# Optimization experiments

Measured on AMD Instinct MI355X. Metric: run time of the kernel, lower is better.

## Reference

```python
import jax, jax.numpy as jnp
import numpy as np
from jax import lax

B, H, W = 2, 960, 1280
K = 1024            # max_keypoints
P = 256             # num_pairs (BAD descriptor dim)
NUM_SCALES = 3
DIFF_ITERS = 3
KAPPA = 0.05
TAU = 0.2           # explicit FED step size (stable < 0.25)
DET_THRESHOLD = 0.001
AKAZE_NMS = 5       # detector-internal NMS window
NMS_WIN = 2 * 3 + 1 # pipeline NMS window (nms_radius=3)
ORI_PATCH = 15
ORI_SIGMA = 2.5
SINK_ITERS = 20
EPSILON = 1.0
UNUSED_SCORE = 1.0
MAX_RADIUS = 5

def _conv(x, k):
    return lax.conv_general_dilated(x, k, (1, 1), 'SAME', dimension_numbers=('NCHW', 'OIHW', 'NCHW'))

_sob = np.array([[-1., 0., 1.], [-2., 0., 2.], [-1., 0., 1.]], np.float32) / 8.0
KX = jnp.asarray(_sob)[None, None]
KY = jnp.asarray(_sob.T)[None, None]
_d2 = np.array([[0., 0., 0.], [1., -2., 1.], [0., 0., 0.]], np.float32)
KXX = jnp.asarray(_d2)[None, None]
KYY = jnp.asarray(_d2.T)[None, None]

# Gaussian weighting kernel for orientation estimation
_c = np.arange(ORI_PATCH, dtype=np.float32) - (ORI_PATCH - 1) / 2.0
_gy, _gx = np.meshgrid(_c, _c, indexing='ij')
_g = np.exp(-(_gx ** 2 + _gy ** 2) / (2.0 * ORI_SIGMA ** 2))
GK = jnp.asarray((_g / _g.sum()).astype(np.float32))[None, None]

# Box-average kernel bank: one normalized box filter per radius 0..MAX_RADIUS
_bc = np.arange(-MAX_RADIUS, MAX_RADIUS + 1, dtype=np.float32)
_by, _bx = np.meshgrid(_bc, _bc, indexing='ij')
_rv = np.arange(MAX_RADIUS + 1, dtype=np.float32)[:, None, None]
_bm = ((np.abs(_by) <= _rv) & (np.abs(_bx) <= _rv)).astype(np.float32)
BOX_BANK = jnp.asarray((_bm / (2.0 * _rv + 1.0) ** 2)[:, None])  # [R+1,1,11,11]

def _shifts(a):
    p = jnp.pad(a, ((0, 0), (0, 0), (1, 1), (1, 1)), mode='edge')
    return p[:, :, :-2, 1:-1], p[:, :, 2:, 1:-1], p[:, :, 1:-1, :-2], p[:, :, 1:-1, 2:]

def _fed_step(L):
    # One explicit Perona-Malik (FED) nonlinear diffusion step
    Lx = _conv(L, KX); Ly = _conv(L, KY)
    g = 1.0 / (1.0 + (Lx * Lx + Ly * Ly) / (KAPPA * KAPPA))
    Ln, Ls, Lw, Le = _shifts(L)
    gn, gs, gw, ge = _shifts(g)
    flux = 0.5 * ((g + gn) * (Ln - L) + (g + gs) * (Ls - L) + (g + gw) * (Lw - L) + (g + ge) * (Le - L))
    return L + TAU * flux

def _maxpool(s, win):
    return lax.reduce_window(s, -jnp.inf, lax.max, (1, win, win), (1, 1, 1), 'SAME')

def _akaze(img):
    # Multi-scale FED diffusion -> Hessian determinant response + orientation map
    L = img
    resp = jnp.zeros((B, H, W), img.dtype)
    for _s in range(NUM_SCALES):
        for _i in range(DIFF_ITERS):
            L = _fed_step(L)
        Lxx = _conv(L, KXX); Lyy = _conv(L, KYY); Lxy = _conv(_conv(L, KX), KY)
        resp = jnp.maximum(resp, (Lxx * Lyy - Lxy * Lxy)[:, 0])
    resp = jnp.where(resp > DET_THRESHOLD, resp, 0.0)
    resp = resp * (resp >= _maxpool(resp, AKAZE_NMS) - 1e-7).astype(resp.dtype)
    gxs = _conv(_conv(img, KX), GK)[:, 0]
    gys = _conv(_conv(img, KY), GK)[:, 0]
    theta = jnp.arctan2(gys, gxs)  # [B,H,W]
    return resp, theta

def _select(resp):
    # Pipeline-level maxpool NMS + top-K selection, pad invalid with (-1,-1)
    mask = (resp >= _maxpool(resp, NMS_WIN) - 1e-7).astype(resp.dtype)
    s = resp * mask
    s = jnp.where(s > 0.0, s, 0.0)
    tk, idx = lax.top_k(s.reshape(B, -1), K)
    y = (idx // W).astype(jnp.float32)
    x = (idx % W).astype(jnp.float32)
    valid = (tk > 0.0).astype(jnp.float32)
    kpts = jnp.where(valid[..., None] > 0.5, jnp.stack([y, x], -1), -1.0)
    return kpts, tk * valid, valid

def _bad(img, kpts, theta, valid, offsets, radii, thresholds):
    # Orientation-aware BAD: box-averaged intensity differences at rotated pair offsets
    bank = _conv(img, BOX_BANK)  # [B,R+1,H,W]
    yc = jnp.clip(kpts[..., 0], 0.0, H - 1.0)
    xc = jnp.clip(kpts[..., 1], 0.0, W - 1.0)
    yi = jnp.round(yc).astype(jnp.int32); xi = jnp.round(xc).astype(jnp.int32)
    th = jax.vmap(lambda m, a, b: m[a, b])(theta, yi, xi)  # [B,K] nearest-sampled orientation
    c = jnp.cos(th)[..., None]; s = jnp.sin(th)[..., None]
    ox1, oy1, ox2, oy2 = offsets[:, 0], offsets[:, 1], offsets[:, 2], offsets[:, 3]
    px1 = xc[..., None] + c * ox1 - s * oy1
    py1 = yc[..., None] + s * ox1 + c * oy1
    px2 = xc[..., None] + c * ox2 - s * oy2
    py2 = yc[..., None] + s * ox2 + c * oy2
    rb = jnp.broadcast_to(radii[None, :], (K, P))
    def samp(px, py):
        xi_ = jnp.clip(jnp.round(px), 0, W - 1).astype(jnp.int32)
        yi_ = jnp.clip(jnp.round(py), 0, H - 1).astype(jnp.int32)
        return jax.vmap(lambda bk, a, b: bk[rb, a, b])(bank, yi_, xi_)  # [B,K,P]
    v = (samp(px1, py1) - samp(px2, py2)) - thresholds[None, None, :]
    v = v * valid[..., None]
    n = jnp.linalg.norm(v, axis=-1, keepdims=True)
    return v / (n + 1e-8)

def _sinkhorn(d1, d2):
    sq1 = jnp.sum(d1 * d1, -1); sq2 = jnp.sum(d2 * d2, -1)
    dist2 = sq1[:, :, None] + sq2[:, None, :] - 2.0 * jnp.einsum('bip,bjp->bij', d1, d2)
    dist = jnp.sqrt(jnp.maximum(dist2, 0.0) + 1e-12)
    Z = jnp.full((B, K + 1, K + 1), UNUSED_SCORE, d1.dtype)
    Z = Z.at[:, :K, :K].set(-dist) / EPSILON
    norm = -jnp.log(2.0 * K)
    log_mu = jnp.concatenate([jnp.zeros(K, Z.dtype), jnp.log(float(K)) * jnp.ones(1, Z.dtype)]) + norm
    log_nu = log_mu
    def body(carry, _):
        u, v = carry
        u = log_mu[None] - jax.nn.logsumexp(Z + v[:, None, :], axis=2)
        v = log_nu[None] - jax.nn.logsumexp(Z + u[:, :, None], axis=1)
        return (u, v), None
    (u, v), _ = lax.scan(body, (jnp.zeros((B, K + 1), Z.dtype), jnp.zeros((B, K + 1), Z.dtype)), None, length=SINK_ITERS)
    return jnp.exp(Z + u[:, :, None] + v[:, None, :] - norm)  # [B,K+1,K+1]

def _forward(img1, img2, offsets, thresholds, radii):
    r1, t1 = _akaze(img1)
    r2, t2 = _akaze(img2)
    k1, s1, v1 = _select(r1)
    k2, s2, v2 = _select(r2)
    d1 = _bad(img1, k1, t1, v1, offsets, radii, thresholds)
    d2 = _bad(img2, k2, t2, v2, offsets, radii, thresholds)
    probs = _sinkhorn(d1, d2)
    return k1, k2, probs

def setup_inputs():
    key = jax.random.key(0)
    k1, k2, k3, k4, k5 = jax.random.split(key, 5)
    img1 = jax.random.uniform(k1, (B, 1, H, W), jnp.float32)
    img2 = jax.random.uniform(k2, (B, 1, H, W), jnp.float32)
    offsets = jax.random.uniform(k3, (P, 4), jnp.float32, -16.0, 16.0)  # box_params - 16
    thresholds = 0.05 * jax.random.normal(k5, (P,), jnp.float32)
    radii = jax.random.randint(k4, (P,), 0, MAX_RADIUS + 1, jnp.int32)
    return {'img1': img1, 'img2': img2, 'offsets': offsets, 'thresholds': thresholds, 'radii': radii}

def reference(img1, img2, offsets, thresholds, radii):
    return _forward(img1, img2, offsets, thresholds, radii)
```

## Files before the change

kernel.cpp:

```cpp
#include <hip/hip_runtime.h>
#include <hip/hip_fp16.h>
#include <math.h>

typedef unsigned long long u64;
typedef unsigned int u32;

#define Hh 960
#define Ww 1280
#define Bb 2
#define Kk 1024
#define Pp 256
#define KP1 1025
#define NSEG 4
#define LISTCAP 131072
#define PR 28
#define PS 57
#define ZLD 1040
static const size_t ZB = (size_t)KP1*ZLD;

static const size_t HWp = (size_t)Hh * Ww;
static const size_t PLn = HWp * Bb;

#define TAUf 0.2f
#define NMS_EPS 1e-7f
#define DET_T 0.001f
#define NORMV (-7.6246189861593985f)
#define LOGKV (6.9314718055994531f)

__constant__ float WR[6] = {1.0f, 1.0f/9.0f, 1.0f/25.0f, 1.0f/49.0f, 1.0f/81.0f, 1.0f/121.0f};

__device__ __forceinline__ int imin(int a,int b){return a<b?a:b;}
__device__ __forceinline__ int imax(int a,int b){return a>b?a:b;}

__global__ __launch_bounds__(256) void fed_step(const float* __restrict__ src, float* __restrict__ dst){
  __shared__ float Lt[36][37];
  __shared__ float Gt[34][35];
  const int bx = blockIdx.x*32, by = blockIdx.y*32, b = blockIdx.z;
  const float* S = src + (size_t)b*HWp;
  float* D = dst + (size_t)b*HWp;
  const int t = threadIdx.y*32 + threadIdx.x;
  for (int i=t;i<36*36;i+=256){
    int ly=i/36, lx=i-ly*36;
    int gy=by+ly-2, gx=bx+lx-2;
    Lt[ly][lx] = (gy>=0 && gy<Hh && gx>=0 && gx<Ww) ? S[(size_t)gy*Ww+gx] : 0.0f;
  }
  __syncthreads();
  const float k2 = (float)(0.05*0.05);
  for (int i=t;i<34*34;i+=256){
    int ly=i/34, lx=i-ly*34;
    int Ly=ly+1, Lx=lx+1;
    float sx = (-Lt[Ly-1][Lx-1]+Lt[Ly-1][Lx+1]
                -2.0f*Lt[Ly][Lx-1]+2.0f*Lt[Ly][Lx+1]
                -Lt[Ly+1][Lx-1]+Lt[Ly+1][Lx+1])*0.125f;
    float sy = (-Lt[Ly-1][Lx-1]-2.0f*Lt[Ly-1][Lx]-Lt[Ly-1][Lx+1]
                +Lt[Ly+1][Lx-1]+2.0f*Lt[Ly+1][Lx]+Lt[Ly+1][Lx+1])*0.125f;
    Gt[ly][lx] = 1.0f/(1.0f + (sx*sx+sy*sy)/k2);
  }
  __syncthreads();
  for (int r=0;r<4;++r){
    int oy=threadIdx.y + r*8, ox=threadIdx.x;
    int gy=by+oy, gx=bx+ox;
    if (gy>=Hh || gx>=Ww) continue;
    int gyn=imax(gy-1,0), gys=imin(gy+1,Hh-1), gxw=imax(gx-1,0), gxe=imin(gx+1,Ww-1);
    float Lc=Lt[oy+2][ox+2];
    float Ln=Lt[gyn-by+2][ox+2];
    float Ls=Lt[gys-by+2][ox+2];
    float Lw=Lt[oy+2][gxw-bx+2];
    float Le=Lt[oy+2][gxe-bx+2];
    float gc=Gt[oy+1][ox+1];
    float gn=Gt[gyn-by+1][ox+1];
    float gs=Gt[gys-by+1][ox+1];
    float gw=Gt[oy+1][gxw-bx+1];
    float ge=Gt[oy+1][gxe-bx+1];
    float flux = 0.5f*((gc+gn)*(Ln-Lc) + (gc+gs)*(Ls-Lc) + (gc+gw)*(Lw-Lc) + (gc+ge)*(Le-Lc));
    D[(size_t)gy*Ww+gx] = Lc + TAUf*flux;
  }
}

__global__ __launch_bounds__(256) void response_kernel(const float* __restrict__ src, float* __restrict__ resp, int first){
  __shared__ float Lt[36][37];
  __shared__ float Sx[34][35];
  const int bx = blockIdx.x*32, by = blockIdx.y*32, b = blockIdx.z;
  const float* S = src + (size_t)b*HWp;
  float* R = resp + (size_t)b*HWp;
  const int t = threadIdx.y*32 + threadIdx.x;
  for (int i=t;i<36*36;i+=256){
    int ly=i/36, lx=i-ly*36;
    int gy=by+ly-2, gx=bx+lx-2;
    Lt[ly][lx] = (gy>=0 && gy<Hh && gx>=0 && gx<Ww) ? S[(size_t)gy*Ww+gx] : 0.0f;
  }
  __syncthreads();
  for (int i=t;i<34*34;i+=256){
    int ly=i/34, lx=i-ly*34;
    int gy=by+ly-1, gx=bx+lx-1;
    float v=0.0f;
    if (gy>=0 && gy<Hh && gx>=0 && gx<Ww){
      int Ly=ly+1, Lx=lx+1;
      v = (-Lt[Ly-1][Lx-1]+Lt[Ly-1][Lx+1]
           -2.0f*Lt[Ly][Lx-1]+2.0f*Lt[Ly][Lx+1]
           -Lt[Ly+1][Lx-1]+Lt[Ly+1][Lx+1])*0.125f;
    }
    Sx[ly][lx]=v;
  }
  __syncthreads();
  for (int r=0;r<4;++r){
    int oy=threadIdx.y + r*8, ox=threadIdx.x;
    int gy=by+oy, gx=bx+ox;
    if (gy>=Hh || gx>=Ww) continue;
    int Ly=oy+2, Lx=ox+2;
    float Lxx = Lt[Ly][Lx-1]-2.0f*Lt[Ly][Lx]+Lt[Ly][Lx+1];
    float Lyy = Lt[Ly-1][Lx]-2.0f*Lt[Ly][Lx]+Lt[Ly+1][Lx];
    int Sy=oy+1, Sxi=ox+1;
    float Lxy = (-Sx[Sy-1][Sxi-1]-2.0f*Sx[Sy-1][Sxi]-Sx[Sy-1][Sxi+1]
                 +Sx[Sy+1][Sxi-1]+2.0f*Sx[Sy+1][Sxi]+Sx[Sy+1][Sxi+1])*0.125f;
    float det = Lxx*Lyy - Lxy*Lxy;
    size_t id=(size_t)gy*Ww+gx;
    R[id] = first ? fmaxf(det,0.0f) : fmaxf(R[id], det);
  }
}

__global__ __launch_bounds__(256) void detect_compact(const float* __restrict__ resp,
                                                      u64* __restrict__ lists,
                                                      int* __restrict__ cnt, int segbase){
  const int TS=42;
  __shared__ float Tt[TS][TS+1];
  __shared__ float H5[TS][40];
  __shared__ float Ss[38][39];
  __shared__ u64 keys[1024];
  __shared__ int lcnt, gbase;
  const int bx = blockIdx.x*32, by = blockIdx.y*32, b = blockIdx.z;
  const float* S = resp + (size_t)b*HWp;
  const int t = threadIdx.y*32 + threadIdx.x;
  if (t==0) lcnt=0;
  for (int i=t;i<TS*TS;i+=256){
    int ly=i/TS, lx=i-ly*TS;
    int gy=by+ly-5, gx=bx+lx-5;
    float v = (gy>=0 && gy<Hh && gx>=0 && gx<Ww) ? S[(size_t)gy*Ww+gx] : 0.0f;
    Tt[ly][lx] = (v>DET_T) ? v : 0.0f;
  }
  __syncthreads();
  for (int i=t;i<42*38;i+=256){
    int y=i/38, x=i-(i/38)*38;
    float m=Tt[y][x];
    m=fmaxf(m,Tt[y][x+1]); m=fmaxf(m,Tt[y][x+2]);
    m=fmaxf(m,Tt[y][x+3]); m=fmaxf(m,Tt[y][x+4]);
    H5[y][x]=m;
  }
  __syncthreads();
  for (int i=t;i<38*38;i+=256){
    int y=i/38, x=i-(i/38)*38;
    float m=H5[y][x];
    m=fmaxf(m,H5[y+1][x]); m=fmaxf(m,H5[y+2][x]);
    m=fmaxf(m,H5[y+3][x]); m=fmaxf(m,H5[y+4][x]);
    float c=Tt[y+2][x+2];
    Ss[y][x]=(c>=m-NMS_EPS)?c:0.0f;
  }
  __syncthreads();
  const int seg=segbase+b;
  for (int r=0;r<4;++r){
    int oy=threadIdx.y + r*8, ox=threadIdx.x;
    int gy=by+oy, gx=bx+ox;
    bool pos=false; u64 key=0;
    if (gy<Hh && gx<Ww){
      float v=Ss[oy+3][ox+3];
      if (v>0.0f){
        float m=0.0f;
        #pragma unroll
        for(int dy=0;dy<7;dy++)
          #pragma unroll
          for(int dx=0;dx<7;dx++)
            m=fmaxf(m,Ss[oy+dy][ox+dx]);
        if (v>=m-NMS_EPS){
          u32 idx=(u32)(gy*Ww+gx);
          key=((u64)__float_as_uint(v)<<32)|(u64)(0xFFFFFFFFu-idx);
          pos=true;
        }
      }
    }
    u64 mask=__ballot(pos);
    if (mask){
      int lane=t&63;
      int leader=__ffsll((long long)mask)-1;
      int base=0;
      if (lane==leader) base=atomicAdd(&lcnt,__popcll(mask));
      base=__shfl(base,leader);
      if (pos){
        int rk=__popcll(mask & ((1ULL<<lane)-1ULL));
        keys[base+rk]=key;
      }
    }
  }
  __syncthreads();
  if (t==0 && lcnt>0) gbase=atomicAdd(&cnt[seg*64], lcnt);
  __syncthreads();
  int n=lcnt;
  for (int i=t;i<n;i+=256){
    int p=gbase+i;
    if (p<LISTCAP) lists[(size_t)seg*LISTCAP+p]=keys[i];
  }
}

__device__ __forceinline__ void segbar(int* bar, int* gen, int seg, int target){
  __syncthreads();
  if(threadIdx.x==0){
    __threadfence();
    int old=atomicAdd(&bar[seg*16],1);
    if(old==7){
      atomicExch(&bar[seg*16],0);
      atomicAdd(&gen[seg*16],1);
    } else {
      while(__hip_atomic_load(&gen[seg*16],__ATOMIC_ACQUIRE,__HIP_MEMORY_SCOPE_AGENT)<target){
        __builtin_amdgcn_s_sleep(8);
      }
    }
    __threadfence();
  }
  __syncthreads();
}

__global__ __launch_bounds__(256) void topk_all(const u64* __restrict__ lists, const int* __restrict__ cnt,
                          u32* __restrict__ ghist, int* __restrict__ krem, int* __restrict__ takeAll,
                          u64* __restrict__ prefix, u64* __restrict__ Tf,
                          u64* __restrict__ selbuf, int* __restrict__ selcnt,
                          int* __restrict__ bar, int* __restrict__ gen){
  const int seg=blockIdx.y, bid=blockIdx.x, tid=threadIdx.x;
  __shared__ u32 h[256];
  __shared__ int tash;
  __shared__ u64 pfxsh;
  const int n=imin(cnt[seg*64],LISTCAP);
  const u64* L=lists+(size_t)seg*LISTCAP;
  int target=0;
  for(int rd=0;rd<8;rd++){
    if(tid==0){
      tash=(rd>0)?__hip_atomic_load(&takeAll[seg],__ATOMIC_RELAXED,__HIP_MEMORY_SCOPE_AGENT):0;
      pfxsh=(rd>0)?__hip_atomic_load(&prefix[seg],__ATOMIC_RELAXED,__HIP_MEMORY_SCOPE_AGENT):0ULL;
    }
    h[tid]=0;
    __syncthreads();
    if(!tash){
      int shift=56-8*rd;
      u64 maskHi=(rd==0)?0ULL:(~0ULL<<(shift+8));
      u64 pfx=pfxsh;
      for(int i=bid*256+tid;i<n;i+=8*256){
        u64 k=L[i];
        if((k&maskHi)==pfx) atomicAdd(&h[(int)((k>>shift)&255ULL)],1u);
      }
      __syncthreads();
      if(h[tid]) atomicAdd(&ghist[seg*256+tid],h[tid]);
    }
    segbar(bar,gen,seg,++target);
    if(bid==0){
      h[tid]=__hip_atomic_load(&ghist[seg*256+tid],__ATOMIC_RELAXED,__HIP_MEMORY_SCOPE_AGENT);
      __syncthreads();
      if(tid==0){
        if(rd==0){
          krem[seg]=Kk;
          __hip_atomic_store(&prefix[seg],0ULL,__ATOMIC_RELEASE,__HIP_MEMORY_SCOPE_AGENT);
          __hip_atomic_store(&takeAll[seg],(n<=Kk)?1:0,__ATOMIC_RELEASE,__HIP_MEMORY_SCOPE_AGENT);
        }
        int taNow=__hip_atomic_load(&takeAll[seg],__ATOMIC_RELAXED,__HIP_MEMORY_SCOPE_AGENT);
        if(taNow){
          if(rd==7) __hip_atomic_store(&Tf[seg],1ULL,__ATOMIC_RELEASE,__HIP_MEMORY_SCOPE_AGENT);
        } else {
          int kr=krem[seg];
          int acc=0,b2=255;
          for(;b2>0;--b2){ int c2=(int)h[b2]; if(acc+c2>=kr) break; acc+=c2; }
          int shift=56-8*rd;
          u64 pf=__hip_atomic_load(&prefix[seg],__ATOMIC_RELAXED,__HIP_MEMORY_SCOPE_AGENT);
          pf|=((u64)(u32)b2)<<shift;
          __hip_atomic_store(&prefix[seg],pf,__ATOMIC_RELEASE,__HIP_MEMORY_SCOPE_AGENT);
          krem[seg]=kr-acc;
          if(rd==7) __hip_atomic_store(&Tf[seg],pf,__ATOMIC_RELEASE,__HIP_MEMORY_SCOPE_AGENT);
        }
      }
      __syncthreads();
      ghist[seg*256+tid]=0u;
    }
    segbar(bar,gen,seg,++target);
  }
  u64 T=__hip_atomic_load(&Tf[seg],__ATOMIC_RELAXED,__HIP_MEMORY_SCOPE_AGENT);
  for(int i0=bid*256;i0<n;i0+=8*256){
    int i=i0+tid;
    bool sel=false; u64 k=0;
    if(i<n){ k=L[i]; sel=(k>=T); }
    u64 mask=__ballot(sel);
    if(mask){
      int lane=tid&63;
      int leader=__ffsll((long long)mask)-1;
      int base=0;
      if(lane==leader) base=atomicAdd(&selcnt[seg*64],__popcll(mask));
      base=__shfl(base,leader);
      if(sel){
        int p=base+__popcll(mask & ((1ULL<<lane)-1ULL));
        if(p<Kk) selbuf[(size_t)seg*Kk+p]=k;
      }
    }
  }
}

__global__ __launch_bounds__(1024) void finalize_kernel(const u64* __restrict__ selbuf, const int* __restrict__ selcnt,
                                int* __restrict__ kyi, int* __restrict__ kxi, float* __restrict__ kval,
                                float* __restrict__ outp){
  int seg=blockIdx.x, tid=threadIdx.x;
  __shared__ u64 a[1024];
  int n=selcnt[seg*64]; if(n>Kk)n=Kk;
  a[tid]=(tid<n)?selbuf[(size_t)seg*Kk+tid]:0ULL;
  __syncthreads();
  for(int k=2;k<=1024;k<<=1){
    for(int j=k>>1;j>0;j>>=1){
      int ixj=tid^j;
      if(ixj>tid){
        u64 x=a[tid], y=a[ixj];
        bool desc=((tid&k)==0);
        if(desc ? (x<y) : (x>y)){ a[tid]=y; a[ixj]=x; }
      }
      __syncthreads();
    }
  }
  u64 key=a[tid];
  bool val=(key!=0ULL);
  u32 idx=0xFFFFFFFFu-(u32)(key&0xFFFFFFFFULL);
  int y= val ? (int)(idx/Ww) : 0;
  int x= val ? (int)(idx%Ww) : 0;
  int mi=seg*Kk+tid;
  kyi[mi]=y; kxi[mi]=x; kval[mi]= val?1.0f:0.0f;
  int imi=seg>>1, bb=seg&1;
  float* ko=outp + (size_t)imi*(Bb*Kk*2) + ((size_t)bb*Kk+tid)*2;
  ko[0]= val ? (float)y : -1.0f;
  ko[1]= val ? (float)x : -1.0f;
}

__global__ void init_weights(float* wn){
  if(threadIdx.x==0 && blockIdx.x==0){
    double w[15]; double S=0.0;
    for(int i=0;i<15;i++){ double c=(double)i-7.0; w[i]=exp(-(c*c)/(2.0*2.5*2.5)); S+=w[i]; }
    for(int i=0;i<15;i++) wn[i]=(float)(w[i]/S);
  }
}

__device__ __forceinline__ float ldz(const float* __restrict__ img,int y,int x){
  return (y>=0&&y<Hh&&x>=0&&x<Ww)?img[(size_t)y*Ww+x]:0.0f;
}

__global__ __launch_bounds__(64) void orient_kernel(const float* __restrict__ img1, const float* __restrict__ img2,
                              const int* __restrict__ kyi, const int* __restrict__ kxi,
                              const float* __restrict__ wn, float* __restrict__ kth){
  int seg=blockIdx.y, ki=blockIdx.x, lane=threadIdx.x;
  __shared__ float w15[15];
  if(lane<15) w15[lane]=wn[lane];
  __syncthreads();
  const float* img=(seg<2?img1:img2)+(size_t)(seg&1)*HWp;
  int mi=seg*Kk+ki;
  int yc=kyi[mi], xc=kxi[mi];
  float ax=0.0f, ay=0.0f;
  for(int tp=lane;tp<225;tp+=64){
    int du=tp/15-7, dv=tp-(tp/15)*15-7;
    int yy=yc+du, xx=xc+dv;
    if(yy<0||yy>=Hh||xx<0||xx>=Ww) continue;
    float p00=ldz(img,yy-1,xx-1), p01=ldz(img,yy-1,xx), p02=ldz(img,yy-1,xx+1);
    float p10=ldz(img,yy,xx-1),                          p12=ldz(img,yy,xx+1);
    float p20=ldz(img,yy+1,xx-1), p21=ldz(img,yy+1,xx), p22=ldz(img,yy+1,xx+1);
    float sx=(-p00+p02-2.0f*p10+2.0f*p12-p20+p22)*0.125f;
    float sy=(-p00-2.0f*p01-p02+p20+2.0f*p21+p22)*0.125f;
    float wgt=w15[du+7]*w15[dv+7];
    ax=fmaf(wgt,sx,ax); ay=fmaf(wgt,sy,ay);
  }
  for(int o=32;o;o>>=1){ ax+=__shfl_down(ax,o); ay+=__shfl_down(ay,o); }
  if(lane==0) kth[mi]=atan2f(ay,ax);
}

__global__ __launch_bounds__(256) void bad_kernel(const float* __restrict__ img1, const float* __restrict__ img2,
                           const float* __restrict__ offs, const float* __restrict__ thrv,
                           const int* __restrict__ rad,
                           const int* __restrict__ kyi, const int* __restrict__ kxi,
                           const float* __restrict__ kval, const float* __restrict__ kth,
                           float* __restrict__ d1, float* __restrict__ d2,
                           float* __restrict__ sq1, float* __restrict__ sq2){
  __shared__ float sat[PS+1][PS+2];
  __shared__ float sm[4];
  __shared__ float nsh;
  int seg=blockIdx.y, ki=blockIdx.x, p=threadIdx.x;
  const float* img=(seg<2?img1:img2)+(size_t)(seg&1)*HWp;
  int mi=seg*Kk+ki;
  int yci=kyi[mi], xci=kxi[mi];
  for (int i=p;i<PS+1;i+=256){ sat[0][i]=0.0f; sat[i][0]=0.0f; }
  if (p==0) sat[0][PS]=0.0f;
  for (int i=p;i<PS*PS;i+=256){
    int ly=i/PS, lx=i-ly*PS;
    int gy=yci-PR+ly, gx=xci-PR+lx;
    sat[ly+1][lx+1]=(gy>=0&&gy<Hh&&gx>=0&&gx<Ww)?img[(size_t)gy*Ww+gx]:0.0f;
  }
  __syncthreads();
  if (p<PS){
    float run=0.0f;
    for(int x=1;x<=PS;x++){ run+=sat[p+1][x]; sat[p+1][x]=run; }
  }
  __syncthreads();
  if (p<PS){
    float run=0.0f;
    for(int y=1;y<=PS;y++){ run+=sat[y][p+1]; sat[y][p+1]=run; }
  }
  __syncthreads();
  float yc=(float)yci, xc=(float)xci;
  float th=kth[mi];
  float c=cosf(th), s=sinf(th);
  float ox1=offs[p*4+0], oy1=offs[p*4+1], ox2=offs[p*4+2], oy2=offs[p*4+3];
  int r=rad[p];
  float w=WR[r];
  float px1=xc+c*ox1-s*oy1, py1=yc+s*ox1+c*oy1;
  float px2=xc+c*ox2-s*oy2, py2=yc+s*ox2+c*oy2;
  auto boxl=[&](float px,float py,int r_)->float{
    float rx=rintf(px), ry=rintf(py);
    int xi=(int)fminf(fmaxf(rx,0.0f),(float)(Ww-1));
    int yi=(int)fminf(fmaxf(ry,0.0f),(float)(Hh-1));
    int lx=xi-(xci-PR), ly=yi-(yci-PR);
    int y2=ly+r_+1, y1=ly-r_, x2=lx+r_+1, x1=lx-r_;
    return sat[y2][x2]-sat[y1][x2]-sat[y2][x1]+sat[y1][x1];
  };
  float s1=boxl(px1,py1,r)*w;
  float s2=boxl(px2,py2,r)*w;
  float v=(s1-s2-thrv[p])*kval[mi];
  float t=v*v;
  for(int o=32;o;o>>=1) t+=__shfl_down(t,o);
  if((p&63)==0) sm[p>>6]=t;
  __syncthreads();
  if(p==0) nsh=sqrtf(sm[0]+sm[1]+sm[2]+sm[3]);
  __syncthreads();
  float dv=v/(nsh+1e-8f);
  float* dd=(seg<2?d1:d2);
  dd[((size_t)(seg&1)*Kk+ki)*Pp+p]=dv;
  float t2=dv*dv;
  for(int o=32;o;o>>=1) t2+=__shfl_down(t2,o);
  __syncthreads();
  if((p&63)==0) sm[p>>6]=t2;
  __syncthreads();
  if(p==0){ float* sq=(seg<2?sq1:sq2); sq[(size_t)(seg&1)*Kk+ki]=sm[0]+sm[1]+sm[2]+sm[3]; }
}

__global__ __launch_bounds__(256) void dist_kernel(const float* __restrict__ d1, const float* __restrict__ d2,
                            const float* __restrict__ sq1, const float* __restrict__ sq2,
                            float* __restrict__ Zm, float* __restrict__ Zt){
  int b=blockIdx.z;
  int i0=blockIdx.y*64, j0=blockIdx.x*64;
  int tid=threadIdx.x;
  int tx=tid&15, ty=tid>>4;
  __shared__ float Ast[64][68], Bst[64][68];
  const float* D1=d1+(size_t)b*Kk*Pp;
  const float* D2=d2+(size_t)b*Kk*Pp;
  float acc[4][4]={};
  for(int p0=0;p0<Pp;p0+=64){
    for(int i=tid;i<64*16;i+=256){
      int row=i>>4, c4=(i&15)<<2;
      float4 va=*reinterpret_cast<const float4*>(&D1[(size_t)(i0+row)*Pp+p0+c4]);
      float4 vb=*reinterpret_cast<const float4*>(&D2[(size_t)(j0+row)*Pp+p0+c4]);
      Ast[c4+0][row]=va.x; Ast[c4+1][row]=va.y; Ast[c4+2][row]=va.z; Ast[c4+3][row]=va.w;
      Bst[c4+0][row]=vb.x; Bst[c4+1][row]=vb.y; Bst[c4+2][row]=vb.z; Bst[c4+3][row]=vb.w;
    }
    __syncthreads();
    #pragma unroll 8
    for(int kk=0;kk<64;++kk){
      float4 av=*reinterpret_cast<const float4*>(&Ast[kk][ty*4]);
      float4 bv=*reinterpret_cast<const float4*>(&Bst[kk][tx*4]);
      acc[0][0]=fmaf(av.x,bv.x,acc[0][0]); acc[0][1]=fmaf(av.x,bv.y,acc[0][1]);
      acc[0][2]=fmaf(av.x,bv.z,acc[0][2]); acc[0][3]=fmaf(av.x,bv.w,acc[0][3]);
      acc[1][0]=fmaf(av.y,bv.x,acc[1][0]); acc[1][1]=fmaf(av.y,bv.y,acc[1][1]);
      acc[1][2]=fmaf(av.y,bv.z,acc[1][2]); acc[1][3]=fmaf(av.y,bv.w,acc[1][3]);
      acc[2][0]=fmaf(av.z,bv.x,acc[2][0]); acc[2][1]=fmaf(av.z,bv.y,acc[2][1]);
      acc[2][2]=fmaf(av.z,bv.z,acc[2][2]); acc[2][3]=fmaf(av.z,bv.w,acc[2][3]);
      acc[3][0]=fmaf(av.w,bv.x,acc[3][0]); acc[3][1]=fmaf(av.w,bv.y,acc[3][1]);
      acc[3][2]=fmaf(av.w,bv.z,acc[3][2]); acc[3][3]=fmaf(av.w,bv.w,acc[3][3]);
    }
    __syncthreads();
  }
  int gi=i0+ty*4, gj=j0+tx*4;
  float si[4], sj[4];
  #pragma unroll
  for(int i=0;i<4;i++){ si[i]=sq1[b*Kk+gi+i]; sj[i]=sq2[b*Kk+gj+i]; }
  #pragma unroll
  for(int i=0;i<4;i++){
    #pragma unroll
    for(int j=0;j<4;j++){
      float dd=si[i]+sj[j]-2.0f*acc[i][j];
      float dist=sqrtf(fmaxf(dd,0.0f)+1e-12f);
      Zm[(size_t)b*ZB+(size_t)(gi+i)*ZLD+(gj+j)]=-dist;
      Zt[(size_t)b*ZB+(size_t)(gj+j)*ZLD+(gi+i)]=-dist;
    }
  }
}

__global__ void zborder_kernel(float* __restrict__ Zm, float* __restrict__ Zt){
  int i=blockIdx.x*256+threadIdx.x;
  if(i>=Bb*KP1) return;
  int b=i/KP1, j=i-(i/KP1)*KP1;
  size_t base=(size_t)b*ZB;
  Zm[base+(size_t)j*ZLD+Kk]=1.0f;
  Zm[base+(size_t)Kk*ZLD+j]=1.0f;
  Zt[base+(size_t)j*ZLD+Kk]=1.0f;
  Zt[base+(size_t)Kk*ZLD+j]=1.0f;
  for(int c=KP1;c<ZLD;c++){
    Zm[base+(size_t)j*ZLD+c]=-1.0e30f;
    Zt[base+(size_t)j*ZLD+c]=-1.0e30f;
  }
}

__global__ void expz_kernel(const float* __restrict__ Zm, const float* __restrict__ Zt,
                            __half* __restrict__ Em, __half* __restrict__ Et){
  size_t q=(size_t)blockIdx.x*256+threadIdx.x;
  const size_t tot4=(size_t)Bb*ZB/4;
  if(q>=2*tot4) return;
  const float* src=(q<tot4)?Zm:Zt;
  __half* dst=(q<tot4)?Em:Et;
  size_t j=(q<tot4)?q:q-tot4;
  float4 z=reinterpret_cast<const float4*>(src)[j];
  __half2 a=__floats2half2_rn(expf(z.x),expf(z.y));
  __half2 b=__floats2half2_rn(expf(z.z),expf(z.w));
  reinterpret_cast<__half2*>(dst)[2*j]=a;
  reinterpret_cast<__half2*>(dst)[2*j+1]=b;
}

__global__ void init_euv(float* __restrict__ euv, float* __restrict__ evv){
  int i=blockIdx.x*256+threadIdx.x;
  if(i>=Bb*ZLD) return;
  int j=i-(i/ZLD)*ZLD;
  evv[i]=(j<KP1)?1.0f:0.0f;
  euv[i]=0.0f;
}

struct H4{ __half2 a, b; };
__global__ __launch_bounds__(256) void sink_gemv(const __half* __restrict__ E,
        const float* __restrict__ evin, float* __restrict__ euout, float* __restrict__ uout){
  int row=blockIdx.x*4+(threadIdx.x>>6);
  if(row>=Bb*KP1) return;
  int b=row/KP1, i=row-b*KP1;
  int lane=threadIdx.x&63;
  const H4* e4=reinterpret_cast<const H4*>(E+((size_t)b*KP1+i)*ZLD);
  const float4* v4=reinterpret_cast<const float4*>(evin+(size_t)b*ZLD);
  float s=0.0f;
  for(int j=lane;j<ZLD/4;j+=64){
    H4 e=e4[j]; float4 v=v4[j];
    float2 ea=__half22float2(e.a), eb=__half22float2(e.b);
    s=fmaf(ea.x,v.x,s); s=fmaf(ea.y,v.y,s);
    s=fmaf(eb.x,v.z,s); s=fmaf(eb.y,v.w,s);
  }
  for(int o=32;o;o>>=1) s+=__shfl_down(s,o);
  if(lane==0){
    float lm,elm;
    if(i<Kk){ lm=NORMV; elm=4.8828125e-4f; }
    else    { lm=LOGKV+NORMV; elm=0.5f; }
    euout[(size_t)b*ZLD+i]=elm/s;
    uout [(size_t)b*ZLD+i]=lm-logf(s);
  }
}

__global__ void probs_kernel(const float* __restrict__ Zm, const float* __restrict__ uu,
                             const float* __restrict__ vv, float* __restrict__ outp){
  size_t i=(size_t)blockIdx.x*256+threadIdx.x;
  const size_t tot=(size_t)Bb*KP1*KP1;
  if(i>=tot) return;
  size_t b=i/((size_t)KP1*KP1);
  size_t rem=i-b*(size_t)KP1*KP1;
  int rr=(int)(rem/KP1), cc=(int)(rem-(size_t)(rem/KP1)*KP1);
  outp[i]=expf(Zm[b*ZB+(size_t)rr*ZLD+cc]+uu[b*ZLD+rr]+vv[b*ZLD+cc]-NORMV);
}

extern "C" void kernel_launch(void* const* d_in, const int* in_sizes, int n_in,
                              void* d_out, int out_size, void* d_ws, size_t ws_size,
                              hipStream_t stream) {
  (void)in_sizes; (void)n_in; (void)out_size;
  const float* img1=(const float*)d_in[0];
  const float* img2=(const float*)d_in[1];
  const float* offs=(const float*)d_in[2];
  const float* thrv=(const float*)d_in[3];
  const int*   rad =(const int*)d_in[4];
  float* out=(float*)d_out;

  const bool batched = ws_size >= ((size_t)72<<20);
  const int NP = batched ? 4 : 2;
  const size_t PB = HWp*(size_t)NP*4;

  char* wp=(char*)d_ws;
  auto carve=[&](size_t bytes)->char*{ char* p=wp; wp += (bytes+255)&~(size_t)255; return p; };
  float* r0  =(float*)carve(PB);
  float* r1  =(float*)carve(PB);
  float* resp=(float*)carve(PB);
  u64*  lists=(u64*)carve((size_t)NSEG*LISTCAP*8);
  char* stateblk = carve(8192);
  int* cnt     =(int*)(stateblk);
  int* selcnt  =(int*)(stateblk+1024);
  int* krem    =(int*)(stateblk+2048);
  int* takeAll =(int*)(stateblk+2112);
  u64* prefix  =(u64*)(stateblk+2176);
  u64* Tf      =(u64*)(stateblk+2240);
  u32* ghist   =(u32*)(stateblk+2304);
  int* bar     =(int*)(stateblk+6656);
  int* gen     =(int*)(stateblk+6912);
  u64* selbuf  =(u64*)carve((size_t)NSEG*Kk*8);
  int* kyi     =(int*)carve((size_t)NSEG*Kk*4);
  int* kxi     =(int*)carve((size_t)NSEG*Kk*4);
  float* kval  =(float*)carve((size_t)NSEG*Kk*4);
  float* kth   =(float*)carve((size_t)NSEG*Kk*4);
  float* d1    =(float*)carve((size_t)Bb*Kk*Pp*4);
  float* d2    =(float*)carve((size_t)Bb*Kk*Pp*4);
  float* sq1   =(float*)carve((size_t)Bb*Kk*4);
  float* sq2   =(float*)carve((size_t)Bb*Kk*4);
  float* uvec  =(float*)carve((size_t)Bb*ZLD*4);
  float* vvec  =(float*)carve((size_t)Bb*ZLD*4);
  float* euvec =(float*)carve((size_t)Bb*ZLD*4);
  float* evvec =(float*)carve((size_t)Bb*ZLD*4);
  float* wn    =(float*)carve(64);

  const size_t EBYTES = ((size_t)Bb*ZB*2 + 255)&~(size_t)255;
  __half* Em=(__half*)resp;
  __half* Et=(__half*)((char*)resp + EBYTES);

  hipMemsetAsync(stateblk, 0, 8192, stream);
  init_weights<<<1,32,0,stream>>>(wn);

  dim3 TB(32,8);
  if (batched){
    dim3 TG(Ww/32, Hh/32, 4);
    hipMemcpyAsync(r0,       img1, PLn*4, hipMemcpyDeviceToDevice, stream);
    hipMemcpyAsync(r0+2*HWp, img2, PLn*4, hipMemcpyDeviceToDevice, stream);
    float* cur=r0; float* oth=r1;
    for(int st=1; st<=9; ++st){
      fed_step<<<TG,TB,0,stream>>>(cur, oth);
      float* tp=cur; cur=oth; oth=tp;
      if(st%3==0) response_kernel<<<TG,TB,0,stream>>>(cur, resp, st==3);
    }
    detect_compact<<<TG,TB,0,stream>>>(resp, lists, cnt, 0);
  } else {
    dim3 TG(Ww/32, Hh/32, Bb);
    for(int im=0; im<2; ++im){
      const float* srcimg = (im==0)? img1 : img2;
      hipMemcpyAsync(r0, srcimg, PLn*4, hipMemcpyDeviceToDevice, stream);
      float* cur=r0; float* oth=r1;
      for(int st=1; st<=9; ++st){
        fed_step<<<TG,TB,0,stream>>>(cur, oth);
        float* tp=cur; cur=oth; oth=tp;
        if(st%3==0) response_kernel<<<TG,TB,0,stream>>>(cur, resp, st==3);
      }
      detect_compact<<<TG,TB,0,stream>>>(resp, lists, cnt, im*2);
    }
  }

  topk_all<<<dim3(8,NSEG),dim3(256),0,stream>>>(lists, cnt, ghist, krem, takeAll,
                                                prefix, Tf, selbuf, selcnt, bar, gen);
  finalize_kernel<<<NSEG,1024,0,stream>>>(selbuf, selcnt, kyi, kxi, kval, out);
  orient_kernel<<<dim3(Kk,NSEG),dim3(64),0,stream>>>(img1, img2, kyi, kxi, wn, kth);
  bad_kernel<<<dim3(Kk,NSEG),dim3(256),0,stream>>>(img1, img2, offs, thrv, rad,
                                                   kyi, kxi, kval, kth, d1, d2, sq1, sq2);

  float* Zm=r0; float* Zt=r1;
  dist_kernel<<<dim3(16,16,Bb),dim3(256),0,stream>>>(d1,d2,sq1,sq2,Zm,Zt);
  zborder_kernel<<<dim3((Bb*KP1+255)/256),dim3(256),0,stream>>>(Zm,Zt);
  {
    size_t tot4=(size_t)Bb*ZB/4;
    expz_kernel<<<dim3((u32)((2*tot4+255)/256)),dim3(256),0,stream>>>(Zm,Zt,Em,Et);
  }
  init_euv<<<dim3((Bb*ZLD+255)/256),dim3(256),0,stream>>>(euvec,evvec);
  for(int it=0; it<20; ++it){
    sink_gemv<<<dim3((Bb*KP1+3)/4),dim3(256),0,stream>>>(Em, evvec, euvec, uvec);
    sink_gemv<<<dim3((Bb*KP1+3)/4),dim3(256),0,stream>>>(Et, euvec, evvec, vvec);
  }
  size_t tot=(size_t)Bb*KP1*KP1;
  probs_kernel<<<dim3((u32)((tot+255)/256)),dim3(256),0,stream>>>(Zm, uvec, vvec, out + (size_t)2*Bb*Kk*2);
}
```

Measured before the change: 655.7 us.

## Replace multi-block top-k with global barriers by one 1024-thread block per segment

The radix-select top-k now runs as a single 1024-thread workgroup per segment instead of eight workgroups coordinated through global atomic barriers and shared global histograms. Histograms, the bin choice (now a parallel suffix scan) and the selection counter all live in shared memory, so the spin-wait barriers and global atomics go away. In exchange, each segment's list scan (up to 131072 keys over eight radix rounds) is done by one workgroup, which cuts the parallelism available for large candidate lists.

```diff
diff --git a/kernel.cpp b/kernel.cpp
--- a/kernel.cpp
+++ b/kernel.cpp
@@ -200,86 +200,58 @@
   }
 }
 
-__device__ __forceinline__ void segbar(int* bar, int* gen, int seg, int target){
-  __syncthreads();
-  if(threadIdx.x==0){
-    __threadfence();
-    int old=atomicAdd(&bar[seg*16],1);
-    if(old==7){
-      atomicExch(&bar[seg*16],0);
-      atomicAdd(&gen[seg*16],1);
-    } else {
-      while(__hip_atomic_load(&gen[seg*16],__ATOMIC_ACQUIRE,__HIP_MEMORY_SCOPE_AGENT)<target){
-        __builtin_amdgcn_s_sleep(8);
-      }
-    }
-    __threadfence();
-  }
-  __syncthreads();
-}
-
-__global__ __launch_bounds__(256) void topk_all(const u64* __restrict__ lists, const int* __restrict__ cnt,
-                          u32* __restrict__ ghist, int* __restrict__ krem, int* __restrict__ takeAll,
-                          u64* __restrict__ prefix, u64* __restrict__ Tf,
-                          u64* __restrict__ selbuf, int* __restrict__ selcnt,
-                          int* __restrict__ bar, int* __restrict__ gen){
-  const int seg=blockIdx.y, bid=blockIdx.x, tid=threadIdx.x;
+__global__ __launch_bounds__(1024) void topk_one(const u64* __restrict__ lists, const int* __restrict__ cnt,
+                                                 u64* __restrict__ selbuf, int* __restrict__ selcnt){
+  const int seg=blockIdx.x, tid=threadIdx.x;
   __shared__ u32 h[256];
-  __shared__ int tash;
-  __shared__ u64 pfxsh;
+  __shared__ u32 scan[256];
+  __shared__ int krem_s, ta_s, bsel, lbase;
+  __shared__ u64 pfx_s;
   const int n=imin(cnt[seg*64],LISTCAP);
   const u64* L=lists+(size_t)seg*LISTCAP;
-  int target=0;
-  for(int rd=0;rd<8;rd++){
-    if(tid==0){
-      tash=(rd>0)?__hip_atomic_load(&takeAll[seg],__ATOMIC_RELAXED,__HIP_MEMORY_SCOPE_AGENT):0;
-      pfxsh=(rd>0)?__hip_atomic_load(&prefix[seg],__ATOMIC_RELAXED,__HIP_MEMORY_SCOPE_AGENT):0ULL;
-    }
-    h[tid]=0;
-    __syncthreads();
-    if(!tash){
+  if(tid==0){ krem_s=Kk; pfx_s=0ULL; ta_s=(n<=Kk)?1:0; lbase=0; }
+  __syncthreads();
+  u64 T=1ULL;
+  if(!ta_s){
+    for(int rd=0;rd<8;rd++){
       int shift=56-8*rd;
       u64 maskHi=(rd==0)?0ULL:(~0ULL<<(shift+8));
-      u64 pfx=pfxsh;
-      for(int i=bid*256+tid;i<n;i+=8*256){
+      u64 pfx=pfx_s;
+      if(tid<256) h[tid]=0;
+      __syncthreads();
+      for(int i=tid;i<n;i+=1024){
         u64 k=L[i];
         if((k&maskHi)==pfx) atomicAdd(&h[(int)((k>>shift)&255ULL)],1u);
       }
       __syncthreads();
-      if(h[tid]) atomicAdd(&ghist[seg*256+tid],h[tid]);
-    }
-    segbar(bar,gen,seg,++target);
-    if(bid==0){
-      h[tid]=__hip_atomic_load(&ghist[seg*256+tid],__ATOMIC_RELAXED,__HIP_MEMORY_SCOPE_AGENT);
+      if(tid<256) scan[tid]=h[tid];
+      __syncthreads();
+      for(int off=1;off<256;off<<=1){
+        u32 v=0;
+        if(tid<256 && tid+off<256) v=scan[tid+off];
+        __syncthreads();
+        if(tid<256) scan[tid]+=v;
+        __syncthreads();
+      }
+      int kr=krem_s;
+      if(tid<256){
+        bool ge=(scan[tid]>=(u32)kr);
+        bool geN=(tid<255)?(scan[tid+1]>=(u32)kr):false;
+        if(ge && !geN) bsel=tid;
+      }
       __syncthreads();
       if(tid==0){
-        if(rd==0){
-          krem[seg]=Kk;
-          __hip_atomic_store(&prefix[seg],0ULL,__ATOMIC_RELEASE,__HIP_MEMORY_SCOPE_AGENT);
-          __hip_atomic_store(&takeAll[seg],(n<=Kk)?1:0,__ATOMIC_RELEASE,__HIP_MEMORY_SCOPE_AGENT);
-        }
-        int taNow=__hip_atomic_load(&takeAll[seg],__ATOMIC_RELAXED,__HIP_MEMORY_SCOPE_AGENT);
-        if(taNow){
-          if(rd==7) __hip_atomic_store(&Tf[seg],1ULL,__ATOMIC_RELEASE,__HIP_MEMORY_SCOPE_AGENT);
-        } else {
-          int kr=krem[seg];
-          int acc=0,b2=255;
-          for(;b2>0;--b2){ int c2=(int)h[b2]; if(acc+c2>=kr) break; acc+=c2; }
-          int shift=56-8*rd;
-          u64 pf=__hip_atomic_load(&prefix[seg],__ATOMIC_RELAXED,__HIP_MEMORY_SCOPE_AGENT);
-          pf|=((u64)(u32)b2)<<shift;
-          __hip_atomic_store(&prefix[seg],pf,__ATOMIC_RELEASE,__HIP_MEMORY_SCOPE_AGENT);
-          krem[seg]=kr-acc;
-          if(rd==7) __hip_atomic_store(&Tf[seg],pf,__ATOMIC_RELEASE,__HIP_MEMORY_SCOPE_AGENT);
-        }
+        int b=bsel;
+        int acc=(b<255)?(int)scan[b+1]:0;
+        pfx_s |= ((u64)(u32)b)<<shift;
+        krem_s = kr-acc;
       }
       __syncthreads();
-      ghist[seg*256+tid]=0u;
-    }
-    segbar(bar,gen,seg,++target);
-  }
-  u64 T=__hip_atomic_load(&Tf[seg],__ATOMIC_RELAXED,__HIP_MEMORY_SCOPE_AGENT);
-  for(int i0=bid*256;i0<n;i0+=8*256){
+    }
+    T=pfx_s;
+  }
+  __syncthreads();
+  for(int i0=0;i0<n;i0+=1024){
     int i=i0+tid;
     bool sel=false; u64 k=0;
     if(i<n){ k=L[i]; sel=(k>=T); }
@@ -288,7 +260,7 @@
       int lane=tid&63;
       int leader=__ffsll((long long)mask)-1;
       int base=0;
-      if(lane==leader) base=atomicAdd(&selcnt[seg*64],__popcll(mask));
+      if(lane==leader) base=atomicAdd(&lbase,__popcll(mask));
       base=__shfl(base,leader);
       if(sel){
         int p=base+__popcll(mask & ((1ULL<<lane)-1ULL));
@@ -296,6 +268,8 @@
       }
     }
   }
+  __syncthreads();
+  if(tid==0) selcnt[seg*64]=imin(lbase,Kk);
 }
 
 __global__ __launch_bounds__(1024) void finalize_kernel(const u64* __restrict__ selbuf, const int* __restrict__ selcnt,
@@ -587,13 +561,6 @@
   char* stateblk = carve(8192);
   int* cnt     =(int*)(stateblk);
   int* selcnt  =(int*)(stateblk+1024);
-  int* krem    =(int*)(stateblk+2048);
-  int* takeAll =(int*)(stateblk+2112);
-  u64* prefix  =(u64*)(stateblk+2176);
-  u64* Tf      =(u64*)(stateblk+2240);
-  u32* ghist   =(u32*)(stateblk+2304);
-  int* bar     =(int*)(stateblk+6656);
-  int* gen     =(int*)(stateblk+6912);
   u64* selbuf  =(u64*)carve((size_t)NSEG*Kk*8);
   int* kyi     =(int*)carve((size_t)NSEG*Kk*4);
   int* kxi     =(int*)carve((size_t)NSEG*Kk*4);
@@ -643,8 +610,7 @@
     }
   }
 
-  topk_all<<<dim3(8,NSEG),dim3(256),0,stream>>>(lists, cnt, ghist, krem, takeAll,
-                                                prefix, Tf, selbuf, selcnt, bar, gen);
+  topk_one<<<dim3(NSEG),dim3(1024),0,stream>>>(lists, cnt, selbuf, selcnt);
   finalize_kernel<<<NSEG,1024,0,stream>>>(selbuf, selcnt, kyi, kxi, kval, out);
   orient_kernel<<<dim3(Kk,NSEG),dim3(64),0,stream>>>(img1, img2, kyi, kxi, wn, kth);
   bad_kernel<<<dim3(Kk,NSEG),dim3(256),0,stream>>>(img1, img2, offs, thrv, rad,
```

Result: faster. 628.2 us (-4.2%).
